# Performance work log

Measured on AMD Instinct MI355X. Metric: run time of the kernel, lower is better.

Reference implementation:

```python
import jax, jax.numpy as jnp
import numpy as np

NODE_DIM = 128; EDGE_DIM = 64; TIME_DIM = 32; HIDDEN = 256; N_LAYERS = 2
K = 20; N_NODES = 100000; B = 8192
IN_DIM = 2 * NODE_DIM + EDGE_DIM + TIME_DIM  # 352


def time2vec(t, w0, b0, w, b):
    # t: [...] -> [..., TIME_DIM]; linear term + sinusoidal terms (Time2Vec)
    t = t[..., None]
    return jnp.concatenate([w0 * t + b0, jnp.sin(w * t + b)], axis=-1)


def msg_mlp(x, W1, b1, W2, b2):
    # TemporalMessageFunction: Linear -> ReLU -> Linear
    return jax.nn.relu(x @ W1 + b1) @ W2 + b2


def gru_cell(x, h, w_ih, w_hh, b_ih, b_hh):
    # torch.nn.GRUCell math, gate order (r, z, n)
    gx = x @ w_ih.T + b_ih
    gh = h @ w_hh.T + b_hh
    rx, zx, nx = jnp.split(gx, 3, axis=-1)
    rh, zh, nh = jnp.split(gh, 3, axis=-1)
    r = jax.nn.sigmoid(rx + rh)
    z = jax.nn.sigmoid(zx + zh)
    n = jnp.tanh(nx + r * nh)
    return (1.0 - z) * n + z * h


def setup_inputs():
    key = jax.random.key(0)
    ks = jax.random.split(key, 24)
    def rn(i, shape, scale=1.0):
        return jax.random.normal(ks[i], shape, dtype=jnp.float32) * scale
    return {
        "src_nodes": jax.random.randint(ks[0], (B,), 0, N_NODES),
        "dst_nodes": jax.random.randint(ks[1], (B,), 0, N_NODES),
        "edge_attrs": rn(2, (B, EDGE_DIM)),
        "timestamps": jax.random.uniform(ks[3], (B,), dtype=jnp.float32) * 1000.0,
        "memory": rn(4, (N_NODES, NODE_DIM), 0.1),
        "neighbor_ids": jax.random.randint(ks[5], (N_NODES, K), 0, N_NODES),
        "neighbor_times": jax.random.uniform(ks[6], (N_NODES, K), dtype=jnp.float32) * 1000.0,
        "neighbor_edge_attrs": rn(7, (N_NODES, K, EDGE_DIM), 0.1),
        "t2v_w0": rn(8, (1,)),
        "t2v_b0": rn(9, (1,)),
        "t2v_w": rn(10, (TIME_DIM - 1,)),
        "t2v_b": rn(11, (TIME_DIM - 1,)),
        "enc_W": rn(12, (EDGE_DIM, EDGE_DIM), EDGE_DIM ** -0.5),
        "enc_b": rn(13, (EDGE_DIM,), 0.01),
        "mlp_W1": rn(14, (N_LAYERS, IN_DIM, HIDDEN), IN_DIM ** -0.5),
        "mlp_b1": rn(15, (N_LAYERS, HIDDEN), 0.01),
        "mlp_W2": rn(16, (N_LAYERS, HIDDEN, NODE_DIM), HIDDEN ** -0.5),
        "mlp_b2": rn(17, (N_LAYERS, NODE_DIM), 0.01),
        "gru_w_ih": rn(18, (3 * NODE_DIM, NODE_DIM), NODE_DIM ** -0.5),
        "gru_w_hh": rn(19, (3 * NODE_DIM, NODE_DIM), NODE_DIM ** -0.5),
        "gru_b_ih": rn(20, (3 * NODE_DIM,), 0.01),
        "gru_b_hh": rn(21, (3 * NODE_DIM,), 0.01),
    }


def reference(src_nodes, dst_nodes, edge_attrs, timestamps, memory,
              neighbor_ids, neighbor_times, neighbor_edge_attrs,
              t2v_w0, t2v_b0, t2v_w, t2v_b, enc_W, enc_b,
              mlp_W1, mlp_b1, mlp_W2, mlp_b2,
              gru_w_ih, gru_w_hh, gru_b_ih, gru_b_hh):
    time_emb = time2vec(timestamps, t2v_w0, t2v_b0, t2v_w, t2v_b)  # [B, T]
    edge_enc = edge_attrs @ enc_W + enc_b                           # [B, E]
    src_emb = memory[src_nodes]                                     # [B, D]
    dst_emb = memory[dst_nodes]                                     # [B, D]

    def neighbor_agg(node_ids, layer):
        # gather K temporal neighbors per node, run message MLP, mean-aggregate
        nb_ids = neighbor_ids[node_ids]                 # [B, K]
        nb_emb = memory[nb_ids]                         # [B, K, D]
        node_mem = jnp.broadcast_to(memory[node_ids][:, None, :], nb_emb.shape)
        nb_t = time2vec(neighbor_times[node_ids], t2v_w0, t2v_b0, t2v_w, t2v_b)  # [B, K, T]
        nb_e = neighbor_edge_attrs[node_ids]            # [B, K, E]
        x = jnp.concatenate([nb_emb, node_mem, nb_e, nb_t], axis=-1)  # [B, K, IN_DIM]
        msgs = msg_mlp(x, mlp_W1[layer], mlp_b1[layer], mlp_W2[layer], mlp_b2[layer])
        return msgs.mean(axis=1)                        # [B, D]

    for l in range(N_LAYERS):
        src_nb = neighbor_agg(src_nodes, l)
        dst_nb = neighbor_agg(dst_nodes, l)
        x_src = jnp.concatenate([src_emb, dst_emb, edge_enc, time_emb], axis=-1)
        x_dst = jnp.concatenate([dst_emb, src_emb, edge_enc, time_emb], axis=-1)
        m_src = msg_mlp(x_src, mlp_W1[l], mlp_b1[l], mlp_W2[l], mlp_b2[l]) + src_nb
        m_dst = msg_mlp(x_dst, mlp_W1[l], mlp_b1[l], mlp_W2[l], mlp_b2[l]) + dst_nb
        src_emb = gru_cell(m_src, src_emb, gru_w_ih, gru_w_hh, gru_b_ih, gru_b_hh)
        dst_emb = gru_cell(m_dst, dst_emb, gru_w_ih, gru_w_hh, gru_b_ih, gru_b_hh)

    return jnp.concatenate([src_emb, dst_emb], axis=-1)  # [B, 2*D]
```

## Files before the change

### kernel.cpp

```cpp
#include <hip/hip_runtime.h>
#include <math.h>


typedef __bf16 bf16;
typedef __bf16 bf16x8 __attribute__((ext_vector_type(8)));
typedef float f32x4 __attribute__((ext_vector_type(4)));

#define MFMA16(a, b, c) __builtin_amdgcn_mfma_f32_16x16x32_bf16((a), (b), (c), 0, 0, 0)

__device__ __forceinline__ void split2(float v, bf16& hi, bf16& lo) {
  hi = (bf16)v;
  lo = (bf16)(v - (float)hi);
}

__device__ __forceinline__ bf16x8 cvt8(const float* __restrict__ p) {
  float4 a = *(const float4*)p;
  float4 b = *(const float4*)(p + 4);
  bf16x8 r;
  r[0] = (bf16)a.x; r[1] = (bf16)a.y; r[2] = (bf16)a.z; r[3] = (bf16)a.w;
  r[4] = (bf16)b.x; r[5] = (bf16)b.y; r[6] = (bf16)b.z; r[7] = (bf16)b.w;
  return r;
}

#define NB_EV 8192
#define ROWS_NB (NB_EV * 20)
#define IN_DIM 352
#define HID 256
#define ND 128

__global__ void k_prep_weights(const float* __restrict__ W1, const float* __restrict__ W2,
                               const float* __restrict__ wih, const float* __restrict__ whh,
                               bf16* __restrict__ W1blk, bf16* __restrict__ W1red,
                               bf16* __restrict__ W2blk,
                               bf16* __restrict__ wihblk, bf16* __restrict__ whhblk,
                               float* __restrict__ w320) {
  const int NW1 = 2 * 11 * 256 * 32;
  const int NW1R = 2 * 7 * 256 * 32;
  const int NW2 = 2 * 2 * 8 * 128 * 32;
  const int NG = 2 * 4 * 384 * 32;
  int total = NW1 + NW1R + NW2 + NG + NG + 512;
  for (int i = blockIdx.x * blockDim.x + threadIdx.x; i < total; i += gridDim.x * blockDim.x) {
    int j = i;
    if (j < NW1) {
      int l = j / 90112, r = j - l * 90112;
      int k0 = r / 8192, r2 = r & 8191;
      int n = r2 >> 5, ko = r2 & 31, k = k0 * 32 + ko;
      W1blk[j] = (bf16)W1[(l * 352 + k) * 256 + n];
    } else if ((j -= NW1) < NW1R) {
      int l = j / 57344, r = j - l * 57344;
      int kq = r / 8192, r2 = r & 8191;
      int n = r2 >> 5, ko = r2 & 31;
      int k = (kq < 4) ? (kq * 32 + ko) : ((kq < 6) ? (256 + (kq - 4) * 32 + ko) : (320 + ko));
      W1red[j] = (bf16)W1[(l * 352 + k) * 256 + n];
    } else if ((j -= NW1R) < NW2) {
      int l = j >> 16, r = j & 65535;
      int plane = r >> 15, r2 = r & 32767;
      int kg = r2 >> 12, r3 = r2 & 4095;
      int n = r3 >> 5, ko = r3 & 31, k = kg * 32 + ko;
      bf16 hi, lo; split2(W2[(l * 256 + k) * 128 + n], hi, lo);
      W2blk[j] = plane ? lo : hi;
    } else if ((j -= NW2) < NG) {
      int plane = j / 49152, r = j - plane * 49152;
      int kg = r / 12288, r2 = r - kg * 12288;
      int n = r2 >> 5, ko = r2 & 31, k = kg * 32 + ko;
      bf16 hi, lo; split2(wih[n * 128 + k], hi, lo);
      wihblk[j] = plane ? lo : hi;
    } else if ((j -= NG) < NG) {
      int plane = j / 49152, r = j - plane * 49152;
      int kg = r / 12288, r2 = r - kg * 12288;
      int n = r2 >> 5, ko = r2 & 31, k = kg * 32 + ko;
      bf16 hi, lo; split2(whh[n * 128 + k], hi, lo);
      whhblk[j] = plane ? lo : hi;
    } else {
      j -= NG;
      int l = j >> 8, n = j & 255;
      w320[j] = W1[(l * 352 + 320) * 256 + n];
    }
  }
}

__global__ void k_prep_misc(const float* __restrict__ ts, const float* __restrict__ w0,
                            const float* __restrict__ b0, const float* __restrict__ w,
                            const float* __restrict__ bb,
                            const int* __restrict__ srcn, const int* __restrict__ dstn,
                            const float* __restrict__ memory,
                            float* __restrict__ time_emb, float* __restrict__ embA0,
                            float* __restrict__ embB0) {
  const int N1 = NB_EV * 32, N2 = NB_EV * ND;
  int total = N1 + N2;
  float w0v = w0[0], b0v = b0[0];
  for (int i = blockIdx.x * blockDim.x + threadIdx.x; i < total; i += gridDim.x * blockDim.x) {
    int j = i;
    if (j < N1) {
      int b = j >> 5, c = j & 31;
      float t = ts[b];
      time_emb[j] = (c == 0) ? (w0v * t + b0v) : sinf(w[c - 1] * t + bb[c - 1]);
    } else {
      j -= N1;
      int b = j >> 7, c = j & 127;
      embA0[j] = memory[(long)srcn[b] * ND + c];
      embB0[j] = memory[(long)dstn[b] * ND + c];
    }
  }
}

__global__ void k_edge(const float* __restrict__ ea, const float* __restrict__ encW,
                       const float* __restrict__ encb, float* __restrict__ out) {
  __shared__ float row[64];
  int b = blockIdx.x, j = threadIdx.x;
  row[j] = ea[b * 64 + j];
  __syncthreads();
  float s = encb[j];
#pragma unroll
  for (int k = 0; k < 64; ++k) s += row[k] * encW[k * 64 + j];
  out[b * 64 + j] = s;
}

__global__ __launch_bounds__(256) void k_hnode(
    const int* __restrict__ srcn, const int* __restrict__ dstn,
    const float* __restrict__ memory, const bf16* __restrict__ W1blk,
    float* __restrict__ Hnode) {
  const int tid = threadIdx.x;
  const int wid = tid >> 6, lane = tid & 63;
  const int colq = lane & 15, cq = lane >> 4;
  const int cq8 = cq * 8;
  const int z = blockIdx.y, layer = z >> 1, side = z & 1;
  const int b0 = blockIdx.x * 64;
  const int* nodes = side ? dstn : srcn;

  long node_r[4];
#pragma unroll
  for (int nr = 0; nr < 4; ++nr) node_r[nr] = nodes[b0 + nr * 16 + colq];

  const bf16* W1l = W1blk + layer * 90112 + 4 * 8192 + (wid * 16 + colq) * 32 + cq8;
  f32x4 acc[4][4];
#pragma unroll
  for (int mc = 0; mc < 4; ++mc)
#pragma unroll
    for (int nr = 0; nr < 4; ++nr) acc[mc][nr] = (f32x4){0.f, 0.f, 0.f, 0.f};
#pragma unroll
  for (int k0 = 0; k0 < 4; ++k0) {
    bf16x8 xb[4];
#pragma unroll
    for (int nr = 0; nr < 4; ++nr)
      xb[nr] = cvt8(memory + node_r[nr] * ND + k0 * 32 + cq8);
    bf16x8 wf[4];
#pragma unroll
    for (int mc = 0; mc < 4; ++mc)
      wf[mc] = *(const bf16x8*)(W1l + k0 * 8192 + mc * 2048);
#pragma unroll
    for (int mc = 0; mc < 4; ++mc)
#pragma unroll
      for (int nr = 0; nr < 4; ++nr)
        acc[mc][nr] = MFMA16(wf[mc], xb[nr], acc[mc][nr]);
  }
#pragma unroll
  for (int mc = 0; mc < 4; ++mc)
#pragma unroll
    for (int nr = 0; nr < 4; ++nr) {
      long row = (long)z * NB_EV + b0 + nr * 16 + colq;
      *(f32x4*)&Hnode[row * 256 + mc * 64 + wid * 16 + cq * 4] = acc[mc][nr];
    }
}

#define HSS2 136
#define F_XS 0
#define F_HHI 35840
#define F_HLO 57600
#define F_CL 79360
#define F_TOT 79680
__global__ __launch_bounds__(256, 2) void k_nbr(
    const int* __restrict__ srcn, const int* __restrict__ dstn,
    const float* __restrict__ memory, const int* __restrict__ nbids,
    const float* __restrict__ nbt, const float* __restrict__ nbe,
    const float* __restrict__ w0p, const float* __restrict__ b0p,
    const float* __restrict__ wp, const float* __restrict__ bp,
    const float* __restrict__ Hnode,
    const bf16* __restrict__ W1red, const bf16* __restrict__ W2blk,
    const float* __restrict__ w320, const float* __restrict__ b1,
    const float* __restrict__ b2, float* __restrict__ nb_out) {
  __shared__ __align__(16) char smem[F_TOT];
  bf16* xs = (bf16*)(smem + F_XS);
  bf16* hhi = (bf16*)(smem + F_HHI);
  bf16* hlo = (bf16*)(smem + F_HLO);
  float* cl = (float*)(smem + F_CL);
  int* nbid_l = (int*)(smem + F_HHI);
  int* flat_l = nbid_l + 80;
  float* t_l = (float*)(flat_l + 80);

  const int tid = threadIdx.x;
  const int wid = tid >> 6, lane = tid & 63;
  const int colq = lane & 15, cq = lane >> 4;
  const int cq8 = cq * 8;
  const int side = blockIdx.y;
  const int r0 = blockIdx.x * 80;
  const int* nodes = side ? dstn : srcn;

  if (tid < 80) {
    int rg = r0 + tid;
    int b = rg / 20, k = rg - b * 20;
    int n = nodes[b];
    int flat = n * 20 + k;
    nbid_l[tid] = nbids[flat];
    flat_l[tid] = flat;
    float t = nbt[flat];
    t_l[tid] = t;
    cl[tid] = w0p[0] * t + b0p[0];
  }
  __syncthreads();

  float clr[5];
  int ev_r[5];
#pragma unroll
  for (int nr = 0; nr < 5; ++nr) {
    int row = nr * 16 + colq;
    clr[nr] = cl[row];
    ev_r[nr] = blockIdx.x * 4 + row / 20;
  }

  for (int task = tid; task < 80 * 56; task += 256) {
    int r = task / 56; int c = (task - r * 56) * 4;
    float4 v;
    if (c < 128) {
      v = *(const float4*)&memory[(long)nbid_l[r] * ND + c];
    } else if (c < 192) {
      v = *(const float4*)&nbe[(long)flat_l[r] * 64 + (c - 128)];
    } else {
      float t = t_l[r];
      float vv[4];
#pragma unroll
      for (int q = 0; q < 4; ++q) {
        int cc = c + q - 192;
        vv[q] = (cc == 0) ? 0.f : __sinf(wp[cc - 1] * t + bp[cc - 1]);
      }
      v = make_float4(vv[0], vv[1], vv[2], vv[3]);
    }
    union { bf16 h[4]; uint2 u; } pk;
    pk.h[0] = (bf16)v.x; pk.h[1] = (bf16)v.y; pk.h[2] = (bf16)v.z; pk.h[3] = (bf16)v.w;
    int swz = (((c & 31) >> 3) ^ (r & 3) ^ ((r >> 2) & 3));
    *(uint2*)&xs[(c >> 5) * 2560 + r * 32 + swz * 8 + (c & 7)] = pk.u;
  }
  __syncthreads();

  const int swzr = cq ^ (colq & 3) ^ ((colq >> 2) & 3);

#pragma unroll
  for (int layer = 0; layer < 2; ++layer) {
    const bf16* W1l = W1red + layer * 57344 + (wid * 16 + colq) * 32 + cq8;
    const float* Hz = Hnode + ((long)(layer * 2 + side) * NB_EV) * 256;

    bf16x8 w1f[7][4];
#pragma unroll
    for (int kq = 0; kq < 7; ++kq)
#pragma unroll
      for (int mc = 0; mc < 4; ++mc)
        w1f[kq][mc] = *(const bf16x8*)(W1l + kq * 8192 + mc * 2048);

    f32x4 acc[4][5];
#pragma unroll
    for (int mc = 0; mc < 4; ++mc)
#pragma unroll
      for (int nr = 0; nr < 5; ++nr)
        acc[mc][nr] = *(const f32x4*)&Hz[(long)ev_r[nr] * 256 + mc * 64 + wid * 16 + cq * 4];

#pragma unroll
    for (int kq = 0; kq < 7; ++kq) {
      bf16x8 xb[5];
#pragma unroll
      for (int nr = 0; nr < 5; ++nr)
        xb[nr] = *(const bf16x8*)(xs + kq * 2560 + (nr * 16 + colq) * 32 + swzr * 8);
#pragma unroll
      for (int mc = 0; mc < 4; ++mc)
#pragma unroll
        for (int nr = 0; nr < 5; ++nr)
          acc[mc][nr] = MFMA16(w1f[kq][mc], xb[nr], acc[mc][nr]);
    }

    const float* w320l = w320 + layer * 256;
    const float* b1l = b1 + layer * 256;
#pragma unroll
    for (int mc = 0; mc < 4; ++mc) {
      int c0 = mc * 64 + wid * 16 + cq * 4;
      float4 wv = *(const float4*)&w320l[c0];
      float4 bv = *(const float4*)&b1l[c0];
#pragma unroll
      for (int nr = 0; nr < 5; ++nr) {
        float c = clr[nr];
        acc[mc][nr][0] = fmaxf(acc[mc][nr][0] + c * wv.x + bv.x, 0.f);
        acc[mc][nr][1] = fmaxf(acc[mc][nr][1] + c * wv.y + bv.y, 0.f);
        acc[mc][nr][2] = fmaxf(acc[mc][nr][2] + c * wv.z + bv.z, 0.f);
        acc[mc][nr][3] = fmaxf(acc[mc][nr][3] + c * wv.w + bv.w, 0.f);
      }
    }

    if (layer == 1) __syncthreads();

    const bf16* W2h = W2blk + layer * 65536 + (wid * 32 + colq) * 32 + cq8;
    const bf16* W2l = W2h + 32768;
    f32x4 acc2[2][5];
#pragma unroll
    for (int mc2 = 0; mc2 < 2; ++mc2)
#pragma unroll
      for (int nr = 0; nr < 5; ++nr) acc2[mc2][nr] = (f32x4){0.f, 0.f, 0.f, 0.f};

#pragma unroll
    for (int hh = 0; hh < 2; ++hh) {
#pragma unroll
      for (int mq = 0; mq < 2; ++mq) {
        int mc = hh * 2 + mq;
        int cl0 = mq * 64 + wid * 16 + cq * 4;
#pragma unroll
        for (int nr = 0; nr < 5; ++nr) {
          int r = nr * 16 + colq;
          union { bf16 h[4]; uint2 u; } ph, pl;
#pragma unroll
          for (int i = 0; i < 4; ++i) split2(acc[mc][nr][i], ph.h[i], pl.h[i]);
          *(uint2*)&hhi[r * HSS2 + cl0] = ph.u;
          *(uint2*)&hlo[r * HSS2 + cl0] = pl.u;
        }
      }
      __syncthreads();

      bf16x8 w2hf[4][2], w2lf[4][2];
#pragma unroll
      for (int kq = 0; kq < 4; ++kq)
#pragma unroll
        for (int mc2 = 0; mc2 < 2; ++mc2) {
          w2hf[kq][mc2] = *(const bf16x8*)(W2h + (hh * 4 + kq) * 4096 + mc2 * 512);
          w2lf[kq][mc2] = *(const bf16x8*)(W2l + (hh * 4 + kq) * 4096 + mc2 * 512);
        }

#pragma unroll
      for (int kq = 0; kq < 4; ++kq) {
        bf16x8 bh[5], bl[5];
#pragma unroll
        for (int nr = 0; nr < 5; ++nr) {
          int r = nr * 16 + colq;
          bh[nr] = *(const bf16x8*)(hhi + r * HSS2 + kq * 32 + cq8);
          bl[nr] = *(const bf16x8*)(hlo + r * HSS2 + kq * 32 + cq8);
        }
#pragma unroll
        for (int mc2 = 0; mc2 < 2; ++mc2)
#pragma unroll
          for (int nr = 0; nr < 5; ++nr) {
            acc2[mc2][nr] = MFMA16(w2hf[kq][mc2], bh[nr], acc2[mc2][nr]);
            acc2[mc2][nr] = MFMA16(w2lf[kq][mc2], bh[nr], acc2[mc2][nr]);
            acc2[mc2][nr] = MFMA16(w2hf[kq][mc2], bl[nr], acc2[mc2][nr]);
          }
      }
      if (hh == 0) __syncthreads();
    }

    {
      const float* b2l = b2 + layer * 128;
      long zbase = (long)(layer * 2 + side) * NB_EV * ND;
#pragma unroll
      for (int e = 0; e < 4; ++e) {
        int lo = e * 20, hi = lo + 20;
        f32x4 v[2];
#pragma unroll
        for (int mc2 = 0; mc2 < 2; ++mc2) {
          v[mc2] = (f32x4){0.f, 0.f, 0.f, 0.f};
#pragma unroll
          for (int nr = 0; nr < 5; ++nr) {
            int rl = nr * 16 + colq;
            if (rl >= lo && rl < hi) v[mc2] += acc2[mc2][nr];
          }
        }
#pragma unroll
        for (int s = 1; s < 16; s <<= 1) {
#pragma unroll
          for (int mc2 = 0; mc2 < 2; ++mc2) {
            v[mc2][0] += __shfl_xor(v[mc2][0], s);
            v[mc2][1] += __shfl_xor(v[mc2][1], s);
            v[mc2][2] += __shfl_xor(v[mc2][2], s);
            v[mc2][3] += __shfl_xor(v[mc2][3], s);
          }
        }
        if (colq == e) {
          long b = blockIdx.x * 4 + e;
#pragma unroll
          for (int mc2 = 0; mc2 < 2; ++mc2) {
            int c = wid * 32 + mc2 * 16 + cq * 4;
            float4 bv = *(const float4*)&b2l[c];
            float4 o;
            o.x = (v[mc2][0] + 20.f * bv.x) * 0.05f;
            o.y = (v[mc2][1] + 20.f * bv.y) * 0.05f;
            o.z = (v[mc2][2] + 20.f * bv.z) * 0.05f;
            o.w = (v[mc2][3] + 20.f * bv.w) * 0.05f;
            *(float4*)&nb_out[zbase + b * ND + c] = o;
          }
        }
      }
    }
  }
}

#define XSS 360
#define HSS 136
#define E_G 46080
#define E_CL 80896
#define E_TOT 81152
__global__ __launch_bounds__(256, 1) void k_event(
    int layer, const float* __restrict__ embA_in, const float* __restrict__ embB_in,
    float* __restrict__ outA, int ostrideA, float* __restrict__ outB, int ostrideB,
    const float* __restrict__ time_emb, const float* __restrict__ edge_enc,
    const bf16* __restrict__ W1blk, const bf16* __restrict__ W2blk,
    const float* __restrict__ w320, const float* __restrict__ b1,
    const float* __restrict__ b2, const float* __restrict__ nb_out,
    const bf16* __restrict__ wihblk, const bf16* __restrict__ whhblk,
    const float* __restrict__ bih, const float* __restrict__ bhh) {
  __shared__ __align__(16) char smem[E_TOT];
  bf16* xs = (bf16*)(smem);
  bf16* hhi = (bf16*)(smem);
  bf16* hlo = (bf16*)(smem + 17408);
  bf16* mhi = (bf16*)(smem);
  bf16* mlo = (bf16*)(smem + 17408);
  bf16* ghi = (bf16*)(smem + E_G);
  bf16* glo = (bf16*)(smem + E_G + 17408);
  float* cl = (float*)(smem + E_CL);

  const int tid = threadIdx.x;
  const int r0 = blockIdx.x * 64;
  const int side = r0 >> 13;
  const int b0r = r0 & (NB_EV - 1);
  const float* ea = side ? embB_in : embA_in;
  const float* eb = side ? embA_in : embB_in;

  if (tid < 64) cl[tid] = time_emb[(b0r + tid) * 32];

  for (int task = tid; task < 64 * 88; task += 256) {
    int r = task / 88; int c = (task - r * 88) * 4;
    int b = b0r + r;
    float4 v;
    if (c < 128) {
      v = *(const float4*)&ea[(long)b * ND + c];
      bf16 h0, l0, h1, l1, h2, l2, h3, l3;
      split2(v.x, h0, l0); split2(v.y, h1, l1); split2(v.z, h2, l2); split2(v.w, h3, l3);
      ghi[r * HSS + c + 0] = h0; glo[r * HSS + c + 0] = l0;
      ghi[r * HSS + c + 1] = h1; glo[r * HSS + c + 1] = l1;
      ghi[r * HSS + c + 2] = h2; glo[r * HSS + c + 2] = l2;
      ghi[r * HSS + c + 3] = h3; glo[r * HSS + c + 3] = l3;
    } else if (c < 256) {
      v = *(const float4*)&eb[(long)b * ND + (c - 128)];
    } else if (c < 320) {
      v = *(const float4*)&edge_enc[(long)b * 64 + (c - 256)];
    } else {
      float vv[4];
#pragma unroll
      for (int q = 0; q < 4; ++q) {
        int cc = c + q - 320;
        vv[q] = (cc == 0) ? 0.f : time_emb[b * 32 + cc];
      }
      v = make_float4(vv[0], vv[1], vv[2], vv[3]);
    }
    union { bf16 h[4]; uint2 u; } pk;
    pk.h[0] = (bf16)v.x; pk.h[1] = (bf16)v.y; pk.h[2] = (bf16)v.z; pk.h[3] = (bf16)v.w;
    *(uint2*)&xs[r * XSS + c] = pk.u;
  }
  __syncthreads();

  const int wid = tid >> 6, lane = tid & 63;
  const int colq = lane & 15, cq = lane >> 4;
  const int rsub = cq * 4;

  const bf16* W1l = W1blk + layer * 90112 + (wid * 64 + colq) * 32 + cq * 8;
  const bf16* xsl = xs + colq * XSS + cq * 8;
  f32x4 acc[4][4];
#pragma unroll
  for (int m = 0; m < 4; ++m)
#pragma unroll
    for (int n = 0; n < 4; ++n) acc[m][n] = (f32x4){0.f, 0.f, 0.f, 0.f};
#pragma unroll
  for (int k0 = 0; k0 < 11; ++k0) {
    bf16x8 a[4], b[4];
#pragma unroll
    for (int m = 0; m < 4; ++m) a[m] = *(const bf16x8*)(xsl + m * 16 * XSS + k0 * 32);
#pragma unroll
    for (int n = 0; n < 4; ++n) b[n] = *(const bf16x8*)(W1l + k0 * 8192 + n * 512);
#pragma unroll
    for (int m = 0; m < 4; ++m)
#pragma unroll
      for (int n = 0; n < 4; ++n) acc[m][n] = MFMA16(a[m], b[n], acc[m][n]);
  }
  __syncthreads();

  const float* w320l = w320 + layer * 256;
  const float* b1l = b1 + layer * 256;
#pragma unroll
  for (int n = 0; n < 4; ++n) {
    int cg = wid * 64 + n * 16 + colq;
    float wv = w320l[cg], bv = b1l[cg];
#pragma unroll
    for (int m = 0; m < 4; ++m)
#pragma unroll
      for (int i = 0; i < 4; ++i) {
        int r = m * 16 + rsub + i;
        acc[m][n][i] = fmaxf(acc[m][n][i] + cl[r] * wv + bv, 0.f);
      }
  }
  if (wid < 2) {
#pragma unroll
    for (int m = 0; m < 4; ++m)
#pragma unroll
      for (int n = 0; n < 4; ++n)
#pragma unroll
        for (int i = 0; i < 4; ++i) {
          int r = m * 16 + rsub + i;
          int cc = wid * 64 + n * 16 + colq;
          bf16 hi, lo; split2(acc[m][n][i], hi, lo);
          hhi[r * HSS + cc] = hi;
          hlo[r * HSS + cc] = lo;
        }
  }
  __syncthreads();

  const bf16* W2h = W2blk + layer * 65536 + (wid * 32 + colq) * 32 + cq * 8;
  const bf16* W2l = W2h + 32768;
  const bf16* hhil = hhi + colq * HSS + cq * 8;
  const bf16* hlol = hlo + colq * HSS + cq * 8;
  f32x4 acc2[4][2];
#pragma unroll
  for (int m = 0; m < 4; ++m)
#pragma unroll
    for (int n = 0; n < 2; ++n) acc2[m][n] = (f32x4){0.f, 0.f, 0.f, 0.f};
#pragma unroll
  for (int kg = 0; kg < 8; ++kg) {
    if (kg == 4) {
      __syncthreads();
      if (wid >= 2) {
#pragma unroll
        for (int m = 0; m < 4; ++m)
#pragma unroll
          for (int n = 0; n < 4; ++n)
#pragma unroll
            for (int i = 0; i < 4; ++i) {
              int r = m * 16 + rsub + i;
              int cc = (wid & 1) * 64 + n * 16 + colq;
              bf16 hi, lo; split2(acc[m][n][i], hi, lo);
              hhi[r * HSS + cc] = hi;
              hlo[r * HSS + cc] = lo;
            }
      }
      __syncthreads();
    }
    int lk = (kg & 3) * 32;
    bf16x8 ahi[4], alo[4], bhi[2], blo[2];
#pragma unroll
    for (int m = 0; m < 4; ++m) {
      ahi[m] = *(const bf16x8*)(hhil + m * 16 * HSS + lk);
      alo[m] = *(const bf16x8*)(hlol + m * 16 * HSS + lk);
    }
#pragma unroll
    for (int n = 0; n < 2; ++n) {
      bhi[n] = *(const bf16x8*)(W2h + kg * 4096 + n * 512);
      blo[n] = *(const bf16x8*)(W2l + kg * 4096 + n * 512);
    }
#pragma unroll
    for (int m = 0; m < 4; ++m)
#pragma unroll
      for (int n = 0; n < 2; ++n) {
        acc2[m][n] = MFMA16(ahi[m], bhi[n], acc2[m][n]);
        acc2[m][n] = MFMA16(ahi[m], blo[n], acc2[m][n]);
        acc2[m][n] = MFMA16(alo[m], bhi[n], acc2[m][n]);
      }
  }
  __syncthreads();

  const float* b2l = b2 + layer * 128;
  const float* nbl = nb_out + ((long)(layer * 2 + side)) * NB_EV * ND;
#pragma unroll
  for (int n = 0; n < 2; ++n) {
    int cg = wid * 32 + n * 16 + colq;
    float bv = b2l[cg];
#pragma unroll
    for (int m = 0; m < 4; ++m)
#pragma unroll
      for (int i = 0; i < 4; ++i) {
        int r = m * 16 + rsub + i;
        float mval = acc2[m][n][i] + bv + nbl[(long)(b0r + r) * ND + cg];
        bf16 hi, lo; split2(mval, hi, lo);
        mhi[r * HSS + cg] = hi;
        mlo[r * HSS + cg] = lo;
      }
  }
  __syncthreads();

  float* outP = side ? outB : outA;
  const int ostride = side ? ostrideB : ostrideA;
  const int rowA = wid * 16 + colq;
  const int rbase = wid * 16 + rsub;
  const bf16* mhil = mhi + rowA * HSS + cq * 8;
  const bf16* mlol = mlo + rowA * HSS + cq * 8;
  const bf16* ghil = ghi + rowA * HSS + cq * 8;
  const bf16* glol = glo + rowA * HSS + cq * 8;
  const bf16* wihl = wihblk + colq * 32 + cq * 8;
  const bf16* whhl = whhblk + colq * 32 + cq * 8;

  for (int jt = 0; jt < 8; ++jt) {
    f32x4 gx[3], gh[3];
#pragma unroll
    for (int g = 0; g < 3; ++g) {
      gx[g] = (f32x4){0.f, 0.f, 0.f, 0.f};
      gh[g] = (f32x4){0.f, 0.f, 0.f, 0.f};
    }
#pragma unroll
    for (int kc = 0; kc < 4; ++kc) {
      bf16x8 amh = *(const bf16x8*)(mhil + kc * 32);
      bf16x8 aml = *(const bf16x8*)(mlol + kc * 32);
      bf16x8 ahh = *(const bf16x8*)(ghil + kc * 32);
      bf16x8 ahl = *(const bf16x8*)(glol + kc * 32);
#pragma unroll
      for (int g = 0; g < 3; ++g) {
        int nb = (g * 128 + jt * 16) * 32;
        bf16x8 bh = *(const bf16x8*)(wihl + kc * 12288 + nb);
        bf16x8 bl = *(const bf16x8*)(wihl + 49152 + kc * 12288 + nb);
        gx[g] = MFMA16(amh, bh, gx[g]);
        gx[g] = MFMA16(aml, bh, gx[g]);
        gx[g] = MFMA16(amh, bl, gx[g]);
        bf16x8 ch = *(const bf16x8*)(whhl + kc * 12288 + nb);
        bf16x8 cl2 = *(const bf16x8*)(whhl + 49152 + kc * 12288 + nb);
        gh[g] = MFMA16(ahh, ch, gh[g]);
        gh[g] = MFMA16(ahl, ch, gh[g]);
        gh[g] = MFMA16(ahh, cl2, gh[g]);
      }
    }
    int j = jt * 16 + colq;
    float bihr = bih[j], bihz = bih[128 + j], bihn = bih[256 + j];
    float bhhr = bhh[j], bhhz = bhh[128 + j], bhhn = bhh[256 + j];
#pragma unroll
    for (int i = 0; i < 4; ++i) {
      int rr = rbase + i;
      float rx = gx[0][i] + bihr, zx = gx[1][i] + bihz, nx = gx[2][i] + bihn;
      float rh = gh[0][i] + bhhr, zh = gh[1][i] + bhhz, nh = gh[2][i] + bhhn;
      float r = 1.f / (1.f + expf(-(rx + rh)));
      float zz = 1.f / (1.f + expf(-(zx + zh)));
      float n = tanhf(nx + r * nh);
      float hval = (float)ghi[rr * HSS + j] + (float)glo[rr * HSS + j];
      outP[(long)(b0r + rr) * ostride + j] = (1.f - zz) * n + zz * hval;
    }
  }
}

extern "C" void kernel_launch(void* const* d_in, const int* in_sizes, int n_in,
                              void* d_out, int out_size, void* d_ws, size_t ws_size,
                              hipStream_t stream) {
  const int* srcn = (const int*)d_in[0];
  const int* dstn = (const int*)d_in[1];
  const float* edge_attrs = (const float*)d_in[2];
  const float* timestamps = (const float*)d_in[3];
  const float* memory = (const float*)d_in[4];
  const int* neighbor_ids = (const int*)d_in[5];
  const float* neighbor_times = (const float*)d_in[6];
  const float* neighbor_edge_attrs = (const float*)d_in[7];
  const float* t2v_w0 = (const float*)d_in[8];
  const float* t2v_b0 = (const float*)d_in[9];
  const float* t2v_w = (const float*)d_in[10];
  const float* t2v_b = (const float*)d_in[11];
  const float* enc_W = (const float*)d_in[12];
  const float* enc_b = (const float*)d_in[13];
  const float* mlp_W1 = (const float*)d_in[14];
  const float* mlp_b1 = (const float*)d_in[15];
  const float* mlp_W2 = (const float*)d_in[16];
  const float* mlp_b2 = (const float*)d_in[17];
  const float* gru_w_ih = (const float*)d_in[18];
  const float* gru_w_hh = (const float*)d_in[19];
  const float* gru_b_ih = (const float*)d_in[20];
  const float* gru_b_hh = (const float*)d_in[21];

  char* ws = (char*)d_ws;
  size_t off = 0;
  auto alloc = [&](size_t bytes) { size_t o = off; off += (bytes + 255) & ~(size_t)255; return o; };
  bf16* W1blk = (bf16*)(ws + alloc((size_t)2 * 11 * 256 * 32 * 2));
  bf16* W1red = (bf16*)(ws + alloc((size_t)2 * 7 * 256 * 32 * 2));
  bf16* W2blk = (bf16*)(ws + alloc((size_t)2 * 2 * 8 * 128 * 32 * 2));
  bf16* wihblk = (bf16*)(ws + alloc((size_t)2 * 4 * 384 * 32 * 2));
  bf16* whhblk = (bf16*)(ws + alloc((size_t)2 * 4 * 384 * 32 * 2));
  float* w320 = (float*)(ws + alloc(512 * 4));
  float* time_emb = (float*)(ws + alloc((size_t)NB_EV * 32 * 4));
  float* edge_enc = (float*)(ws + alloc((size_t)NB_EV * 64 * 4));
  float* embA0 = (float*)(ws + alloc((size_t)NB_EV * ND * 4));
  float* embB0 = (float*)(ws + alloc((size_t)NB_EV * ND * 4));
  float* embA1 = (float*)(ws + alloc((size_t)NB_EV * ND * 4));
  float* embB1 = (float*)(ws + alloc((size_t)NB_EV * ND * 4));
  float* nb_out = (float*)(ws + alloc((size_t)4 * NB_EV * ND * 4));
  float* Hnode = (float*)(ws + alloc((size_t)4 * NB_EV * 256 * 4));

  k_prep_weights<<<512, 256, 0, stream>>>(mlp_W1, mlp_W2, gru_w_ih, gru_w_hh,
                                          W1blk, W1red, W2blk, wihblk, whhblk, w320);
  k_prep_misc<<<1024, 256, 0, stream>>>(timestamps, t2v_w0, t2v_b0, t2v_w, t2v_b,
                                        srcn, dstn, memory, time_emb, embA0, embB0);
  k_edge<<<NB_EV, 64, 0, stream>>>(edge_attrs, enc_W, enc_b, edge_enc);
  k_hnode<<<dim3(128, 4, 1), 256, 0, stream>>>(srcn, dstn, memory, W1blk, Hnode);

  k_nbr<<<dim3(ROWS_NB / 80, 2, 1), 256, 0, stream>>>(
      srcn, dstn, memory, neighbor_ids, neighbor_times, neighbor_edge_attrs,
      t2v_w0, t2v_b0, t2v_w, t2v_b, Hnode, W1red, W2blk, w320, mlp_b1, mlp_b2, nb_out);

  k_event<<<2 * NB_EV / 64, 256, 0, stream>>>(
      0, embA0, embB0, embA1, ND, embB1, ND, time_emb, edge_enc,
      W1blk, W2blk, w320, mlp_b1, mlp_b2, nb_out,
      wihblk, whhblk, gru_b_ih, gru_b_hh);

  float* outf = (float*)d_out;
  k_event<<<2 * NB_EV / 64, 256, 0, stream>>>(
      1, embA1, embB1, outf, 2 * ND, outf + ND, 2 * ND, time_emb, edge_enc,
      W1blk, W2blk, w320, mlp_b1, mlp_b2, nb_out,
      wihblk, whhblk, gru_b_ih, gru_b_hh);
}
```

Baseline: 588.1 us.

## Pre-convert neighbor features to bf16 in separate prep kernels before k_nbr

Adds a kernel that converts the whole node memory table to bf16 and another that gathers neighbor edge attributes and time2vec features into a linear bf16 buffer, along with neighbor ids and linear time terms. k_nbr then loads 16-byte bf16 vectors instead of converting fp32 gathers inline, aiming to halve gather bandwidth and simplify its staging loop. It also reorders the accumulator and weight loads and adds empty asm barriers to pin weight registers. The cost is an extra full pass over the 100k-node memory table and an intermediate buffer write and read.

```diff
diff --git a/kernel.cpp b/kernel.cpp
--- a/kernel.cpp
+++ b/kernel.cpp
@@ -24,6 +24,7 @@
 
 #define NB_EV 8192
 #define ROWS_NB (NB_EV * 20)
+#define N_NODES 100000
 #define IN_DIM 352
 #define HID 256
 #define ND 128
@@ -104,6 +105,56 @@
   }
 }
 
+__global__ void k_prep_mem(const float* __restrict__ memory, bf16* __restrict__ memB) {
+  long total = (long)N_NODES * ND / 8;
+  for (long i = blockIdx.x * blockDim.x + threadIdx.x; i < total; i += (long)gridDim.x * blockDim.x) {
+    bf16x8 v = cvt8(memory + i * 8);
+    *(bf16x8*)&memB[i * 8] = v;
+  }
+}
+
+__global__ __launch_bounds__(256) void k_prep_nbr(
+    const int* __restrict__ srcn, const int* __restrict__ dstn,
+    const int* __restrict__ nbids, const float* __restrict__ nbt,
+    const float* __restrict__ nbe,
+    const float* __restrict__ w0p, const float* __restrict__ b0p,
+    const float* __restrict__ wp, const float* __restrict__ bp,
+    bf16* __restrict__ Xlin, int* __restrict__ nbidArr, float* __restrict__ clArr) {
+  __shared__ int flat_l[64];
+  __shared__ float t_l[64];
+  const int tid = threadIdx.x;
+  const int side = blockIdx.y;
+  const int r0 = blockIdx.x * 64;
+  const int* nodes = side ? dstn : srcn;
+  if (tid < 64) {
+    int rg = r0 + tid;
+    int b = rg / 20, k = rg - b * 20;
+    int n = nodes[b];
+    int flat = n * 20 + k;
+    flat_l[tid] = flat;
+    nbidArr[side * ROWS_NB + rg] = nbids[flat];
+    float t = nbt[flat];
+    t_l[tid] = t;
+    clArr[side * ROWS_NB + rg] = w0p[0] * t + b0p[0];
+  }
+  __syncthreads();
+  for (int task = tid; task < 64 * 12; task += 256) {
+    int r = task / 12, j = task - r * 12;
+    bf16x8 v;
+    if (j < 8) {
+      v = cvt8(nbe + (long)flat_l[r] * 64 + j * 8);
+    } else {
+      float t = t_l[r];
+#pragma unroll
+      for (int q = 0; q < 8; ++q) {
+        int c = (j - 8) * 8 + q;
+        v[q] = (c == 0) ? (bf16)0.f : (bf16)__sinf(wp[c - 1] * t + bp[c - 1]);
+      }
+    }
+    *(bf16x8*)&Xlin[((long)side * ROWS_NB + r0 + r) * 96 + j * 8] = v;
+  }
+}
+
 __global__ void k_edge(const float* __restrict__ ea, const float* __restrict__ encW,
                        const float* __restrict__ encb, float* __restrict__ out) {
   __shared__ float row[64];
@@ -170,11 +221,8 @@
 #define F_CL 79360
 #define F_TOT 79680
 __global__ __launch_bounds__(256, 2) void k_nbr(
-    const int* __restrict__ srcn, const int* __restrict__ dstn,
-    const float* __restrict__ memory, const int* __restrict__ nbids,
-    const float* __restrict__ nbt, const float* __restrict__ nbe,
-    const float* __restrict__ w0p, const float* __restrict__ b0p,
-    const float* __restrict__ wp, const float* __restrict__ bp,
+    const bf16* __restrict__ memB, const int* __restrict__ nbidArr,
+    const float* __restrict__ clArr, const bf16* __restrict__ Xlin,
     const float* __restrict__ Hnode,
     const bf16* __restrict__ W1red, const bf16* __restrict__ W2blk,
     const float* __restrict__ w320, const float* __restrict__ b1,
@@ -185,8 +233,6 @@
   bf16* hlo = (bf16*)(smem + F_HLO);
   float* cl = (float*)(smem + F_CL);
   int* nbid_l = (int*)(smem + F_HHI);
-  int* flat_l = nbid_l + 80;
-  float* t_l = (float*)(flat_l + 80);
 
   const int tid = threadIdx.x;
   const int wid = tid >> 6, lane = tid & 63;
@@ -194,18 +240,10 @@
   const int cq8 = cq * 8;
   const int side = blockIdx.y;
   const int r0 = blockIdx.x * 80;
-  const int* nodes = side ? dstn : srcn;
 
   if (tid < 80) {
-    int rg = r0 + tid;
-    int b = rg / 20, k = rg - b * 20;
-    int n = nodes[b];
-    int flat = n * 20 + k;
-    nbid_l[tid] = nbids[flat];
-    flat_l[tid] = flat;
-    float t = nbt[flat];
-    t_l[tid] = t;
-    cl[tid] = w0p[0] * t + b0p[0];
+    nbid_l[tid] = nbidArr[side * ROWS_NB + r0 + tid];
+    cl[tid] = clArr[side * ROWS_NB + r0 + tid];
   }
   __syncthreads();
 
@@ -218,27 +256,21 @@
     ev_r[nr] = blockIdx.x * 4 + row / 20;
   }
 
-  for (int task = tid; task < 80 * 56; task += 256) {
-    int r = task / 56; int c = (task - r * 56) * 4;
-    float4 v;
-    if (c < 128) {
-      v = *(const float4*)&memory[(long)nbid_l[r] * ND + c];
-    } else if (c < 192) {
-      v = *(const float4*)&nbe[(long)flat_l[r] * 64 + (c - 128)];
+  for (int task = tid; task < 80 * 28; task += 256) {
+    int r = task / 28, c16 = task - r * 28;
+    bf16x8 v;
+    int kq, k8;
+    if (c16 < 16) {
+      v = *(const bf16x8*)&memB[(long)nbid_l[r] * ND + c16 * 8];
+      kq = c16 >> 2; k8 = c16 & 3;
     } else {
-      float t = t_l[r];
-      float vv[4];
-#pragma unroll
-      for (int q = 0; q < 4; ++q) {
-        int cc = c + q - 192;
-        vv[q] = (cc == 0) ? 0.f : __sinf(wp[cc - 1] * t + bp[cc - 1]);
-      }
-      v = make_float4(vv[0], vv[1], vv[2], vv[3]);
-    }
-    union { bf16 h[4]; uint2 u; } pk;
-    pk.h[0] = (bf16)v.x; pk.h[1] = (bf16)v.y; pk.h[2] = (bf16)v.z; pk.h[3] = (bf16)v.w;
-    int swz = (((c & 31) >> 3) ^ (r & 3) ^ ((r >> 2) & 3));
-    *(uint2*)&xs[(c >> 5) * 2560 + r * 32 + swz * 8 + (c & 7)] = pk.u;
+      int jj = c16 - 16;
+      v = *(const bf16x8*)&Xlin[((long)side * ROWS_NB + r0 + r) * 96 + jj * 8];
+      kq = (jj < 8) ? (4 + (jj >> 2)) : 6;
+      k8 = (jj < 8) ? (jj & 3) : (jj - 8);
+    }
+    int swz = k8 ^ (r & 3) ^ ((r >> 2) & 3);
+    *(bf16x8*)&xs[kq * 2560 + r * 32 + swz * 8] = v;
   }
   __syncthreads();
 
@@ -249,19 +281,24 @@
     const bf16* W1l = W1red + layer * 57344 + (wid * 16 + colq) * 32 + cq8;
     const float* Hz = Hnode + ((long)(layer * 2 + side) * NB_EV) * 256;
 
+    f32x4 acc[4][5];
+#pragma unroll
+    for (int mc = 0; mc < 4; ++mc)
+#pragma unroll
+      for (int nr = 0; nr < 5; ++nr)
+        acc[mc][nr] = *(const f32x4*)&Hz[(long)ev_r[nr] * 256 + mc * 64 + wid * 16 + cq * 4];
+
     bf16x8 w1f[7][4];
 #pragma unroll
     for (int kq = 0; kq < 7; ++kq)
 #pragma unroll
       for (int mc = 0; mc < 4; ++mc)
         w1f[kq][mc] = *(const bf16x8*)(W1l + kq * 8192 + mc * 2048);
-
-    f32x4 acc[4][5];
-#pragma unroll
-    for (int mc = 0; mc < 4; ++mc)
-#pragma unroll
-      for (int nr = 0; nr < 5; ++nr)
-        acc[mc][nr] = *(const f32x4*)&Hz[(long)ev_r[nr] * 256 + mc * 64 + wid * 16 + cq * 4];
+#pragma unroll
+    for (int kq = 0; kq < 7; ++kq)
+#pragma unroll
+      for (int mc = 0; mc < 4; ++mc)
+        asm volatile("" : "+v"(w1f[kq][mc]));
 
 #pragma unroll
     for (int kq = 0; kq < 7; ++kq) {
@@ -328,6 +365,13 @@
         for (int mc2 = 0; mc2 < 2; ++mc2) {
           w2hf[kq][mc2] = *(const bf16x8*)(W2h + (hh * 4 + kq) * 4096 + mc2 * 512);
           w2lf[kq][mc2] = *(const bf16x8*)(W2l + (hh * 4 + kq) * 4096 + mc2 * 512);
+        }
+#pragma unroll
+      for (int kq = 0; kq < 4; ++kq)
+#pragma unroll
+        for (int mc2 = 0; mc2 < 2; ++mc2) {
+          asm volatile("" : "+v"(w2hf[kq][mc2]));
+          asm volatile("" : "+v"(w2lf[kq][mc2]));
         }
 
 #pragma unroll
@@ -685,17 +729,24 @@
   float* embB1 = (float*)(ws + alloc((size_t)NB_EV * ND * 4));
   float* nb_out = (float*)(ws + alloc((size_t)4 * NB_EV * ND * 4));
   float* Hnode = (float*)(ws + alloc((size_t)4 * NB_EV * 256 * 4));
+  bf16* memB = (bf16*)(ws + alloc((size_t)N_NODES * ND * 2));
+  bf16* Xlin = (bf16*)(ws + alloc((size_t)2 * ROWS_NB * 96 * 2));
+  int* nbidArr = (int*)(ws + alloc((size_t)2 * ROWS_NB * 4));
+  float* clArr = (float*)(ws + alloc((size_t)2 * ROWS_NB * 4));
 
   k_prep_weights<<<512, 256, 0, stream>>>(mlp_W1, mlp_W2, gru_w_ih, gru_w_hh,
                                           W1blk, W1red, W2blk, wihblk, whhblk, w320);
   k_prep_misc<<<1024, 256, 0, stream>>>(timestamps, t2v_w0, t2v_b0, t2v_w, t2v_b,
                                         srcn, dstn, memory, time_emb, embA0, embB0);
+  k_prep_mem<<<2048, 256, 0, stream>>>(memory, memB);
+  k_prep_nbr<<<dim3(2560, 2, 1), 256, 0, stream>>>(
+      srcn, dstn, neighbor_ids, neighbor_times, neighbor_edge_attrs,
+      t2v_w0, t2v_b0, t2v_w, t2v_b, Xlin, nbidArr, clArr);
   k_edge<<<NB_EV, 64, 0, stream>>>(edge_attrs, enc_W, enc_b, edge_enc);
   k_hnode<<<dim3(128, 4, 1), 256, 0, stream>>>(srcn, dstn, memory, W1blk, Hnode);
 
   k_nbr<<<dim3(ROWS_NB / 80, 2, 1), 256, 0, stream>>>(
-      srcn, dstn, memory, neighbor_ids, neighbor_times, neighbor_edge_attrs,
-      t2v_w0, t2v_b0, t2v_w, t2v_b, Hnode, W1red, W2blk, w320, mlp_b1, mlp_b2, nb_out);
+      memB, nbidArr, clArr, Xlin, Hnode, W1red, W2blk, w320, mlp_b1, mlp_b2, nb_out);
 
   k_event<<<2 * NB_EV / 64, 256, 0, stream>>>(
       0, embA0, embB0, embA1, ND, embB1, ND, time_emb, edge_enc,
```

Result: faster. 529.7 us (-9.9%).
